# Kernel tuning notes

Hardware: AMD Instinct MI355X
Metric: run time of the kernel (lower is better)

## Reference

```python
import jax, jax.numpy as jnp
import numpy as np

N = 50000
E = 800000
G = 64
H, C = 16, 4  # heads, out_channels per head; H*C = 64


def setup_inputs() -> dict:
    key = jax.random.key(0)
    ks = jax.random.split(key, 16)
    return {
        "x": jax.random.normal(ks[0], (N,), jnp.float32),
        "edge_index": jax.random.randint(ks[1], (2, E), 0, N),
        "edge_attr": jax.random.normal(ks[2], (E,), jnp.float32),
        "batch": jnp.sort(jax.random.randint(ks[3], (N,), 0, G)),
        # GATv2Conv(1 -> 4, heads=16, edge_dim=1, concat=True)
        "Wl": jax.random.normal(ks[4], (1, H * C), jnp.float32) * 0.5,
        "bl": jnp.full((H * C,), 0.01, jnp.float32),
        "Wr": jax.random.normal(ks[5], (1, H * C), jnp.float32) * 0.5,
        "br": jnp.full((H * C,), 0.01, jnp.float32),
        "We": jax.random.normal(ks[6], (1, H * C), jnp.float32) * 0.5,
        "att": jax.random.normal(ks[7], (H, C), jnp.float32) * 0.5,
        "gat_bias": jnp.zeros((H * C,), jnp.float32),
        # GraphNorm(64)
        "gn_w": jnp.ones((H * C,), jnp.float32),
        "gn_b": jnp.zeros((H * C,), jnp.float32),
        "gn_ms": jnp.ones((H * C,), jnp.float32),
        # SAGEConv(64 -> 64, mean aggr, root weight)
        "sage_Wl": jax.random.normal(ks[8], (H * C, 64), jnp.float32) * 0.125,
        "sage_bl": jnp.full((64,), 0.01, jnp.float32),
        "sage_Wr": jax.random.normal(ks[9], (H * C, 64), jnp.float32) * 0.125,
        # MLP head
        "fc1_W": jax.random.normal(ks[10], (128, 2048), jnp.float32) * 0.08,
        "fc1_b": jnp.full((2048,), 0.01, jnp.float32),
        "fc2_W": jax.random.normal(ks[11], (2048, 1024), jnp.float32) * 0.02,
        "fc2_b": jnp.full((1024,), 0.01, jnp.float32),
        "fc3_W": jax.random.normal(ks[12], (1024, 3), jnp.float32) * 0.03,
        "fc3_b": jnp.full((3,), 0.01, jnp.float32),
    }


def reference(x, edge_index, edge_attr, batch, Wl, bl, Wr, br, We, att, gat_bias,
              gn_w, gn_b, gn_ms, sage_Wl, sage_bl, sage_Wr,
              fc1_W, fc1_b, fc2_W, fc2_b, fc3_W, fc3_b):
    src0, dst0 = edge_index[0], edge_index[1]
    x1 = x[:, None]  # [N,1] (torch.unsqueeze(x, -1))
    # ---- GATv2Conv ----
    xl = (x1 @ Wl + bl).reshape(N, H, C)  # source-side (x_j, also the value)
    xr = (x1 @ Wr + br).reshape(N, H, C)  # target-side (x_i)
    # add self loops; fill_value='mean' -> per-node mean of incoming edge_attr
    deg_in = jax.ops.segment_sum(jnp.ones((E,), x.dtype), dst0, num_segments=N)
    loop_attr = jax.ops.segment_sum(edge_attr, dst0, num_segments=N) / jnp.maximum(deg_in, 1.0)
    loops = jnp.arange(N)
    src = jnp.concatenate([src0, loops])
    dst = jnp.concatenate([dst0, loops])
    ea = jnp.concatenate([edge_attr, loop_attr])[:, None]  # [E+N,1]
    e = (ea @ We).reshape(-1, H, C)
    m = jax.nn.leaky_relu(xl[src] + xr[dst] + e, 0.2)  # [E+N,H,C]
    score = jnp.einsum('ehc,hc->eh', m, att)
    smax = jax.ops.segment_max(score, dst, num_segments=N)
    a = jnp.exp(score - smax[dst])
    denom = jax.ops.segment_sum(a, dst, num_segments=N)
    alpha = a / denom[dst]  # segmented softmax over incoming edges
    h = jax.ops.segment_sum(alpha[:, :, None] * xl[src], dst, num_segments=N)
    h = h.reshape(N, H * C) + gat_bias
    h = jax.nn.relu(h)
    # ---- GraphNorm ----
    cnt = jax.ops.segment_sum(jnp.ones((N,), x.dtype), batch, num_segments=G)[:, None]
    mean = jax.ops.segment_sum(h, batch, num_segments=G) / cnt
    o = h - mean[batch] * gn_ms
    var = jax.ops.segment_sum(o * o, batch, num_segments=G) / cnt
    h = gn_w * o / jnp.sqrt(var[batch] + 1e-5) + gn_b
    # ---- SAGEConv (mean aggregation + root weight) ----
    neigh = jax.ops.segment_sum(h[src0], dst0, num_segments=N) / jnp.maximum(deg_in, 1.0)[:, None]
    h = neigh @ sage_Wl + sage_bl + h @ sage_Wr
    h = jax.nn.relu(h)
    # ---- global max + mean pooling, MLP head (eval mode: dropout off) ----
    gmax = jax.ops.segment_max(h, batch, num_segments=G)
    gmean = jax.ops.segment_sum(h, batch, num_segments=G) / cnt
    g = jnp.concatenate([gmax, gmean], axis=1)  # [G, 128]
    g = jax.nn.relu(g @ fc1_W + fc1_b)
    g = jax.nn.relu(g @ fc2_W + fc2_b)
    return g @ fc3_W + fc3_b
```

## Files before the change

kernel.cpp:

```cpp
#include <hip/hip_runtime.h>

#define GG 64
#define HH 16
#define KK 64

__device__ __forceinline__ float bf2f(unsigned short u){
  return __uint_as_float(((unsigned)u) << 16);
}
__device__ __forceinline__ unsigned short f2bf(float f){
  unsigned u = __float_as_uint(f);
  unsigned r = u + 0x7fffu + ((u >> 16) & 1u);
  return (unsigned short)(r >> 16);
}

__global__ void k_zero(int4* __restrict__ p, int nInt4,
                       const int* __restrict__ batch, int N, int* __restrict__ goff){
  int t = blockIdx.x*blockDim.x + threadIdx.x;
  for (int i = t; i < nInt4; i += gridDim.x*blockDim.x)
    p[i] = make_int4(0,0,0,0);
  if (blockIdx.x == 0 && threadIdx.x <= GG){
    int g = threadIdx.x;
    int lo = 0, hi = N;
    while (lo < hi){ int mid = (lo+hi) >> 1; if (batch[mid] < g) lo = mid+1; else hi = mid; }
    goff[g] = lo;
  }
}


__global__ void k_count_rank(const int* __restrict__ ei, int* deg, int* __restrict__ rank, int E){
  int e = blockIdx.x*blockDim.x + threadIdx.x;
  if (e < E) rank[e] = atomicAdd(&deg[ei[E + e]], 1);
}

__global__ void k_scanA(const int* __restrict__ deg, int* __restrict__ bsum,
                        int* __restrict__ counter, int* __restrict__ row_start_N,
                        int N, int NB){
  int tid = threadIdx.x;
  int base = blockIdx.x*1024;
  int lim = min(base + 1024, N);
  int s = 0;
  for (int i = base + tid; i < lim; i += 256) s += deg[i];
  #pragma unroll
  for (int ofs = 32; ofs >= 1; ofs >>= 1) s += __shfl_down(s, ofs, 64);
  __shared__ int ws[4];
  __shared__ int lastflag;
  int lane = tid & 63, wv = tid >> 6;
  if (lane == 0) ws[wv] = s;
  __syncthreads();
  if (tid == 0){
    bsum[blockIdx.x] = ws[0] + ws[1] + ws[2] + ws[3];
    __threadfence();
    int d = atomicAdd(counter, 1);
    lastflag = (d == NB - 1);
  }
  __syncthreads();
  if (!lastflag) return;
  __threadfence();
  if (NB <= 64){
    if (tid < 64){
      int v = (tid < NB) ? bsum[tid] : 0;
      int val = v;
      #pragma unroll
      for (int ofs = 1; ofs < 64; ofs <<= 1){
        int tt = __shfl_up(val, ofs, 64);
        if ((tid & 63) >= ofs) val += tt;
      }
      if (tid < NB) bsum[tid] = val - v;
      if (tid == NB - 1) *row_start_N = val;
    }
  } else if (tid == 0){
    int run = 0;
    for (int i = 0; i < NB; ++i){ int tmp = bsum[i]; bsum[i] = run; run += tmp; }
    *row_start_N = run;
  }
}

__global__ void k_scan3(const int* __restrict__ deg, const int* __restrict__ bsum,
                        int* __restrict__ row_start, int N){
  int b = blockIdx.x;
  int base = b*1024 + (int)threadIdx.x*4;
  int d0 = (base+0 < N) ? deg[base+0] : 0;
  int d1 = (base+1 < N) ? deg[base+1] : 0;
  int d2 = (base+2 < N) ? deg[base+2] : 0;
  int d3 = (base+3 < N) ? deg[base+3] : 0;
  int s = d0 + d1 + d2 + d3;
  int lane = threadIdx.x & 63, wv = threadIdx.x >> 6;
  int val = s;
  #pragma unroll
  for (int ofs = 1; ofs < 64; ofs <<= 1){
    int tt = __shfl_up(val, ofs, 64);
    if (lane >= ofs) val += tt;
  }
  __shared__ int ws[4];
  if (lane == 63) ws[wv] = val;
  __syncthreads();
  if (threadIdx.x == 0){
    int run = 0;
    #pragma unroll
    for (int w = 0; w < 4; ++w){ int tmp = ws[w]; ws[w] = run; run += tmp; }
  }
  __syncthreads();
  int pre = bsum[b] + ws[wv] + val - s;
  if (base+0 < N){ row_start[base+0] = pre; pre += d0; }
  if (base+1 < N){ row_start[base+1] = pre; pre += d1; }
  if (base+2 < N){ row_start[base+2] = pre; pre += d2; }
  if (base+3 < N){ row_start[base+3] = pre; }
}

__global__ void k_scatter(const int* __restrict__ ei, const float* __restrict__ ea,
                          const int* __restrict__ row_start, const int* __restrict__ rank,
                          unsigned* __restrict__ cs, int E){
  int e = blockIdx.x*blockDim.x + threadIdx.x;
  if (e >= E) return;
  int d = ei[E + e];
  int pos = row_start[d] + rank[e];
  cs[pos] = ((unsigned)ei[e] & 0xFFFFu) | ((unsigned)f2bf(ea[e]) << 16);
}

__global__ void k_gat(const float* __restrict__ x, const int* __restrict__ row_start,
                      const unsigned* __restrict__ cs,
                      const float* __restrict__ Wl, const float* __restrict__ bl,
                      const float* __restrict__ Wr, const float* __restrict__ br,
                      const float* __restrict__ We, const float* __restrict__ att,
                      const float* __restrict__ gat_bias, const int* __restrict__ batch,
                      float* __restrict__ h, float* __restrict__ gsum, float* __restrict__ gsum2,
                      int N){
  __shared__ float sh[32][KK+1];
  __shared__ int bg[32];
  int tid = threadIdx.x;
  int t = blockIdx.x*blockDim.x + tid;
  int n   = t >> 3;
  int sub = t & 7;
  int u   = tid >> 3;
  bool act = (n < N);
  if (sub == 0) bg[u] = act ? batch[n] : -1;
  int k0 = sub*8;
  if (act){
    float xd = x[n];
    float wl[8], we[8], at[8], pre[8];
    #pragma unroll
    for (int i = 0; i < 8; ++i){
      int k = k0 + i;
      wl[i] = Wl[k]; we[i] = We[k]; at[i] = att[k];
      pre[i] = bl[k] + fmaf(xd, Wr[k], br[k]);
    }
    int e0 = row_start[n], e1 = row_start[n+1];
    float m[2]  = {-3.4e38f,-3.4e38f};
    float den[2] = {0,0}, S1[2] = {0,0};
    float asum = 0.f;

#define PROC(XS, EAV)                                                        \
    { float xs_ = (XS), ea_ = (EAV);                                         \
      _Pragma("unroll")                                                      \
      for (int hi2 = 0; hi2 < 2; ++hi2){                                     \
        float sc = 0.f;                                                      \
        _Pragma("unroll")                                                    \
        for (int c = 0; c < 4; ++c){                                         \
          int i = hi2*4 + c;                                                 \
          float tt = fmaf(xs_, wl[i], fmaf(ea_, we[i], pre[i]));             \
          tt = (tt > 0.f) ? tt : 0.2f*tt;                                    \
          sc = fmaf(tt, at[i], sc);                                          \
        }                                                                    \
        float nm = fmaxf(m[hi2], sc);                                        \
        float corr = __expf(m[hi2] - nm);                                    \
        float a    = __expf(sc - nm);                                        \
        den[hi2] = den[hi2]*corr + a;                                        \
        S1[hi2]  = S1[hi2] *corr + a*xs_;                                    \
        m[hi2] = nm; } }

    int e = e0;
    for (; e + 3 < e1; e += 4){
      unsigned w0 = cs[e], w1 = cs[e+1], w2 = cs[e+2], w3 = cs[e+3];
      float xs0 = x[w0 & 0xFFFFu], xs1 = x[w1 & 0xFFFFu];
      float xs2 = x[w2 & 0xFFFFu], xs3 = x[w3 & 0xFFFFu];
      float ea0 = bf2f((unsigned short)(w0 >> 16)), ea1 = bf2f((unsigned short)(w1 >> 16));
      float ea2 = bf2f((unsigned short)(w2 >> 16)), ea3 = bf2f((unsigned short)(w3 >> 16));
      asum += (ea0 + ea1) + (ea2 + ea3);
      PROC(xs0, ea0);
      PROC(xs1, ea1);
      PROC(xs2, ea2);
      PROC(xs3, ea3);
    }
    for (; e < e1; ++e){
      unsigned w0 = cs[e];
      float xs0 = x[w0 & 0xFFFFu], ea0 = bf2f((unsigned short)(w0 >> 16));
      asum += ea0;
      PROC(xs0, ea0);
    }
    {
      float degf = (float)(e1 - e0);
      float eav = asum / fmaxf(degf, 1.0f);
      PROC(xd, eav);
    }
#undef PROC
    #pragma unroll
    for (int hi2 = 0; hi2 < 2; ++hi2){
      float r = S1[hi2] / den[hi2];
      float4 o;
      #pragma unroll
      for (int c = 0; c < 4; ++c){
        int i = hi2*4 + c, k = k0 + i;
        float v = fmaxf(fmaf(wl[i], r, bl[k] + gat_bias[k]), 0.f);
        ((float*)&o)[c] = v;
        sh[u][k] = v;
      }
      *(float4*)(h + (size_t)n*KK + k0 + hi2*4) = o;
    }
  } else {
    #pragma unroll
    for (int i = 0; i < 8; ++i) sh[u][k0+i] = 0.f;
  }
  __syncthreads();
  int ch = tid & 63, slice = tid >> 6;
  int cg = -2; float rs = 0.f, rs2 = 0.f;
  for (int uu = slice*8; uu < slice*8 + 8; ++uu){
    int g = bg[uu];
    if (g != cg){
      if (cg >= 0){ atomicAdd(&gsum[cg*KK + ch], rs); atomicAdd(&gsum2[cg*KK + ch], rs2); }
      cg = g; rs = 0.f; rs2 = 0.f;
    }
    if (g >= 0){ float v = sh[uu][ch]; rs += v; rs2 += v*v; }
  }
  if (cg >= 0){ atomicAdd(&gsum[cg*KK + ch], rs); atomicAdd(&gsum2[cg*KK + ch], rs2); }
}

__global__ void k_norm(float* __restrict__ h, unsigned short* __restrict__ hb,
                       const int* __restrict__ batch,
                       const float* __restrict__ gsum, const float* __restrict__ gsum2,
                       const int* __restrict__ goff,
                       const float* __restrict__ gn_w, const float* __restrict__ gn_b,
                       const float* __restrict__ gn_ms, int N){
  int t = blockIdx.x*blockDim.x + threadIdx.x;
  if (t >= N*16) return;
  int n = t >> 4, q = t & 15;
  int b = batch[n];
  float c = fmaxf((float)(goff[b+1] - goff[b]), 1.0f);
  float inv = 1.0f / c;
  float4 hv = *(float4*)(h + (size_t)n*KK + q*4);
  float ov[4];
  #pragma unroll
  for (int i = 0; i < 4; ++i){
    int k = q*4 + i;
    float mean = gsum[b*KK + k]*inv;
    float eh2  = gsum2[b*KK + k]*inv;
    float ms = gn_ms[k];
    float var = eh2 - 2.f*ms*mean*mean + ms*ms*mean*mean;
    float sc = gn_w[k] * __frsqrt_rn(var + 1e-5f);
    float sh = gn_b[k] - sc*mean*ms;
    ov[i] = fmaf(sc, ((float*)&hv)[i], sh);
  }
  *(float4*)(h + (size_t)n*KK + q*4) = make_float4(ov[0], ov[1], ov[2], ov[3]);
  ushort4 bv;
  bv.x = f2bf(ov[0]); bv.y = f2bf(ov[1]); bv.z = f2bf(ov[2]); bv.w = f2bf(ov[3]);
  *(ushort4*)(hb + (size_t)n*KK + q*4) = bv;
}

__global__ void k_sage(const float* __restrict__ h, const unsigned short* __restrict__ hb,
                       const int* __restrict__ row_start, const unsigned* __restrict__ cs,
                       const float* __restrict__ Wl, const float* __restrict__ bln,
                       const float* __restrict__ Wr, const int* __restrict__ batch,
                       unsigned* __restrict__ gmaxu, float* __restrict__ gsumP, int N){
  __shared__ float snm[16][KK], shn[16][KK];
  __shared__ int bg[16];
  const ushort4* hb4 = (const ushort4*)hb;
  int tid = threadIdx.x;
  int u = tid >> 4;
  int q = tid & 15;
  int n = blockIdx.x*16 + u;
  if (tid < 16) bg[tid] = (blockIdx.x*16 + tid < N) ? batch[blockIdx.x*16 + tid] : -1;
  if (n < N){
    int e0 = row_start[n], e1 = row_start[n+1];
    float a0=0.f,a1=0.f,a2=0.f,a3=0.f;
    float b0=0.f,b1=0.f,b2=0.f,b3=0.f;
    int e = e0;
    for (; e + 7 < e1; e += 8){
      int s0 = cs[e]   & 0xFFFF, s1 = cs[e+1] & 0xFFFF, s2 = cs[e+2] & 0xFFFF, s3 = cs[e+3] & 0xFFFF;
      int s4 = cs[e+4] & 0xFFFF, s5 = cs[e+5] & 0xFFFF, s6 = cs[e+6] & 0xFFFF, s7 = cs[e+7] & 0xFFFF;
      ushort4 v0 = hb4[(size_t)s0*16 + q];
      ushort4 v1 = hb4[(size_t)s1*16 + q];
      ushort4 v2 = hb4[(size_t)s2*16 + q];
      ushort4 v3 = hb4[(size_t)s3*16 + q];
      ushort4 v4 = hb4[(size_t)s4*16 + q];
      ushort4 v5 = hb4[(size_t)s5*16 + q];
      ushort4 v6 = hb4[(size_t)s6*16 + q];
      ushort4 v7 = hb4[(size_t)s7*16 + q];
      a0 += bf2f(v0.x); a1 += bf2f(v0.y); a2 += bf2f(v0.z); a3 += bf2f(v0.w);
      b0 += bf2f(v1.x); b1 += bf2f(v1.y); b2 += bf2f(v1.z); b3 += bf2f(v1.w);
      a0 += bf2f(v2.x); a1 += bf2f(v2.y); a2 += bf2f(v2.z); a3 += bf2f(v2.w);
      b0 += bf2f(v3.x); b1 += bf2f(v3.y); b2 += bf2f(v3.z); b3 += bf2f(v3.w);
      a0 += bf2f(v4.x); a1 += bf2f(v4.y); a2 += bf2f(v4.z); a3 += bf2f(v4.w);
      b0 += bf2f(v5.x); b1 += bf2f(v5.y); b2 += bf2f(v5.z); b3 += bf2f(v5.w);
      a0 += bf2f(v6.x); a1 += bf2f(v6.y); a2 += bf2f(v6.z); a3 += bf2f(v6.w);
      b0 += bf2f(v7.x); b1 += bf2f(v7.y); b2 += bf2f(v7.z); b3 += bf2f(v7.w);
    }
    if (e + 3 < e1){
      int s0 = cs[e] & 0xFFFF, s1 = cs[e+1] & 0xFFFF, s2 = cs[e+2] & 0xFFFF, s3 = cs[e+3] & 0xFFFF;
      ushort4 v0 = hb4[(size_t)s0*16 + q];
      ushort4 v1 = hb4[(size_t)s1*16 + q];
      ushort4 v2 = hb4[(size_t)s2*16 + q];
      ushort4 v3 = hb4[(size_t)s3*16 + q];
      a0 += bf2f(v0.x); a1 += bf2f(v0.y); a2 += bf2f(v0.z); a3 += bf2f(v0.w);
      b0 += bf2f(v1.x); b1 += bf2f(v1.y); b2 += bf2f(v1.z); b3 += bf2f(v1.w);
      a0 += bf2f(v2.x); a1 += bf2f(v2.y); a2 += bf2f(v2.z); a3 += bf2f(v2.w);
      b0 += bf2f(v3.x); b1 += bf2f(v3.y); b2 += bf2f(v3.z); b3 += bf2f(v3.w);
      e += 4;
    }
    for (; e < e1; ++e){
      ushort4 v0 = hb4[(size_t)(cs[e] & 0xFFFF)*16 + q];
      a0 += bf2f(v0.x); a1 += bf2f(v0.y); a2 += bf2f(v0.z); a3 += bf2f(v0.w);
    }
    float dg = fmaxf((float)(e1 - e0), 1.0f);
    float inv = 1.0f/dg;
    float4 nm = make_float4((a0+b0)*inv, (a1+b1)*inv, (a2+b2)*inv, (a3+b3)*inv);
    *(float4*)&snm[u][q*4] = nm;
    *(float4*)&shn[u][q*4] = *(const float4*)(h + (size_t)n*KK + q*4);
  }
  __syncthreads();
  int j = tid & 63, u0 = tid >> 6;
  float acc[4];
  #pragma unroll
  for (int p = 0; p < 4; ++p) acc[p] = bln[j];
  for (int k = 0; k < KK; ++k){
    float wlv = Wl[k*KK + j], wrv = Wr[k*KK + j];
    #pragma unroll
    for (int p = 0; p < 4; ++p){
      int un = u0 + p*4;
      acc[p] = fmaf(snm[un][k], wlv, acc[p]);
      acc[p] = fmaf(shn[un][k], wrv, acc[p]);
    }
  }
  __syncthreads();
  #pragma unroll
  for (int p = 0; p < 4; ++p)
    snm[u0 + p*4][j] = fmaxf(acc[p], 0.f);
  __syncthreads();
  if (tid < 64){
    int cg = -2; float rmax = 0.f, rsum = 0.f;
    for (int uu = 0; uu < 16; ++uu){
      int g = bg[uu];
      if (g != cg){
        if (cg >= 0){
          atomicMax(&gmaxu[cg*KK + tid], __float_as_uint(rmax));
          atomicAdd(&gsumP[cg*KK + tid], rsum);
        }
        cg = g; rmax = 0.f; rsum = 0.f;
      }
      if (g >= 0){ float v = snm[uu][tid]; rmax = fmaxf(rmax, v); rsum += v; }
    }
    if (cg >= 0){
      atomicMax(&gmaxu[cg*KK + tid], __float_as_uint(rmax));
      atomicAdd(&gsumP[cg*KK + tid], rsum);
    }
  }
}


__global__ void k_fc1(const unsigned* __restrict__ gmaxu, const float* __restrict__ gsumP,
                      const int* __restrict__ goff,
                      const float* __restrict__ W, const float* __restrict__ b,
                      float* __restrict__ out){
  __shared__ float sin[128];
  int g = blockIdx.y, jt = blockIdx.x;
  int tid = threadIdx.x;
  if (tid < 128){
    float c = fmaxf((float)(goff[g+1] - goff[g]), 1.0f);
    sin[tid] = (tid < 64) ? __uint_as_float(gmaxu[g*64 + tid])
                          : gsumP[g*64 + (tid-64)] / c;
  }
  __syncthreads();
  int j = jt*256 + tid;
  float acc = b[j];
  #pragma unroll 16
  for (int k = 0; k < 128; ++k)
    acc = fmaf(sin[k], W[(size_t)k*2048 + j], acc);
  out[(size_t)g*2048 + j] = fmaxf(acc, 0.f);
}

__global__ void k_fc2a(const float* __restrict__ in, const float* __restrict__ W,
                       float* __restrict__ partial){
  __shared__ float sin[64][128];
  int jt = blockIdx.x, ks = blockIdx.y;
  int k0 = ks*128;
  int tid = threadIdx.x;
  for (int idx = tid; idx < 64*128; idx += 256){
    int g = idx >> 7, k = idx & 127;
    sin[g][k] = in[(size_t)g*2048 + k0 + k];
  }
  __syncthreads();
  int j = tid & 63, gs = tid >> 6;
  const float* Wp = W + (size_t)k0*1024 + jt*64 + j;
  float acc[16];
  #pragma unroll
  for (int p = 0; p < 16; ++p) acc[p] = 0.f;
  for (int k = 0; k < 128; ++k){
    float w = Wp[(size_t)k*1024];
    #pragma unroll
    for (int p = 0; p < 16; ++p)
      acc[p] = fmaf(sin[gs*16 + p][k], w, acc[p]);
  }
  #pragma unroll
  for (int p = 0; p < 16; ++p){
    int g = gs*16 + p;
    partial[((size_t)ks*64 + g)*1024 + jt*64 + j] = acc[p];
  }
}

__global__ void k_fc2red(const float* __restrict__ partial, const float* __restrict__ b,
                         float* __restrict__ out){
  int i = blockIdx.x*blockDim.x + threadIdx.x;
  int g = i >> 10, j = i & 1023;
  float s = b[j];
  #pragma unroll
  for (int ks = 0; ks < 16; ++ks)
    s += partial[((size_t)ks*64 + g)*1024 + j];
  out[i] = fmaxf(s, 0.f);
}

__global__ void k_fc3(const float* __restrict__ in, const float* __restrict__ W,
                      const float* __restrict__ b, float* __restrict__ out, int nOut){
  int w = (blockIdx.x*blockDim.x + threadIdx.x) >> 6;
  int lane = threadIdx.x & 63;
  if (w >= GG*nOut) return;
  int g = w / nOut, j = w - g*nOut;
  const float* row = in + (size_t)g*1024;
  float acc = 0.f;
  #pragma unroll
  for (int k = lane; k < 1024; k += 64)
    acc = fmaf(row[k], W[(size_t)k*nOut + j], acc);
  #pragma unroll
  for (int ofs = 32; ofs >= 1; ofs >>= 1)
    acc += __shfl_down(acc, ofs, 64);
  if (lane == 0) out[w] = acc + b[j];
}

extern "C" void kernel_launch(void* const* d_in, const int* in_sizes, int n_in,
                              void* d_out, int out_size, void* d_ws, size_t ws_size,
                              hipStream_t stream) {
  const float* x        = (const float*)d_in[0];
  const int*   ei       = (const int*)d_in[1];
  const float* ea       = (const float*)d_in[2];
  const int*   batch    = (const int*)d_in[3];
  const float* Wl       = (const float*)d_in[4];
  const float* bl       = (const float*)d_in[5];
  const float* Wr       = (const float*)d_in[6];
  const float* br       = (const float*)d_in[7];
  const float* We       = (const float*)d_in[8];
  const float* att      = (const float*)d_in[9];
  const float* gat_bias = (const float*)d_in[10];
  const float* gn_w     = (const float*)d_in[11];
  const float* gn_b     = (const float*)d_in[12];
  const float* gn_ms    = (const float*)d_in[13];
  const float* sage_Wl  = (const float*)d_in[14];
  const float* sage_bl  = (const float*)d_in[15];
  const float* sage_Wr  = (const float*)d_in[16];
  const float* fc1_W    = (const float*)d_in[17];
  const float* fc1_b    = (const float*)d_in[18];
  const float* fc2_W    = (const float*)d_in[19];
  const float* fc2_b    = (const float*)d_in[20];
  const float* fc3_W    = (const float*)d_in[21];
  const float* fc3_b    = (const float*)d_in[22];

  const int N = in_sizes[0];
  const int E = in_sizes[1] / 2;
  const int NB = (N + 1023) / 1024;

  char* ws = (char*)d_ws;
  size_t off = 0;
  auto alloc = [&](size_t bytes){ void* p = ws + off; off += (bytes + 255) & ~(size_t)255; return p; };

  int*      deg_i  = (int*)alloc((size_t)N*4);
  float*    gsum   = (float*)alloc(GG*KK*4);
  float*    gsum2  = (float*)alloc(GG*KK*4);
  unsigned* gmaxu  = (unsigned*)alloc(GG*KK*4);
  float*    gsumP  = (float*)alloc(GG*KK*4);
  int*      counter= (int*)alloc(256);
  size_t zero_bytes = off;
  int*   rank      = (int*)alloc((size_t)E*4);
  int*   bsum      = (int*)alloc((size_t)NB*4);
  int*   row_start = (int*)alloc((size_t)(N+1)*4);
  int*   goff      = (int*)alloc((GG+1)*4);
  unsigned* csp    = (unsigned*)alloc((size_t)E*4);
  float* h         = (float*)alloc((size_t)N*KK*4);
  unsigned short* hb = (unsigned short*)alloc((size_t)N*KK*2);
  float* out1      = (float*)alloc((size_t)GG*2048*4);
  float* out2      = (float*)alloc((size_t)GG*1024*4);
  float* partial   = (float*)alloc((size_t)16*GG*1024*4);
  (void)ws_size; (void)n_in; (void)out_size;

  const int B = 256;
  {
    int nInt4 = (int)(zero_bytes >> 4);
    int blocks = min((nInt4 + B - 1)/B, 256);
    k_zero <<<blocks, B, 0, stream>>>((int4*)d_ws, nInt4, batch, N, goff);
  }
  k_count_rank<<<(E+B-1)/B, B, 0, stream>>>(ei, deg_i, rank, E);
  k_scanA  <<<NB, B, 0, stream>>>(deg_i, bsum, counter, row_start + N, N, NB);
  k_scan3  <<<NB, B, 0, stream>>>(deg_i, bsum, row_start, N);
  k_scatter<<<(E+B-1)/B, B, 0, stream>>>(ei, ea, row_start, rank, csp, E);
  k_gat    <<<((size_t)N*8+B-1)/B, B, 0, stream>>>(x, row_start, csp,
                                                   Wl, bl, Wr, br, We, att, gat_bias,
                                                   batch, h, gsum, gsum2, N);
  k_norm   <<<((size_t)N*16+B-1)/B, B, 0, stream>>>(h, hb, batch, gsum, gsum2, goff,
                                                    gn_w, gn_b, gn_ms, N);
  k_sage   <<<(N+15)/16, B, 0, stream>>>(h, hb, row_start, csp, sage_Wl, sage_bl, sage_Wr,
                                         batch, gmaxu, gsumP, N);
  {
    dim3 grid(8, GG);
    k_fc1  <<<grid, 256, 0, stream>>>(gmaxu, gsumP, goff, fc1_W, fc1_b, out1);
  }
  {
    dim3 grid(16, 16);
    k_fc2a <<<grid, 256, 0, stream>>>(out1, fc2_W, partial);
  }
  k_fc2red <<<(GG*1024+B-1)/B, B, 0, stream>>>(partial, fc2_b, out2);
  k_fc3    <<<(GG*3*64+B-1)/B, B, 0, stream>>>(out2, fc3_W, fc3_b, (float*)d_out, 3);
}
```

Baseline: 179.2 us.

## Fuse scan into single-pass look-back and merge fc2 split-K with reduction

Replaces the two-kernel prefix scan with one kernel using a decoupled look-back over per-block status flags. Replaces the split-K fc2 plus separate reduction kernel with a single kernel that loops over the full K dimension and applies bias and ReLU in place. This removes two launches and the partial buffer traffic, but fc2 now runs only 64 blocks and re-reads the weight matrix once per group slice. The look-back also relies on forward progress of earlier blocks.

```diff
diff --git a/kernel.cpp b/kernel.cpp
--- a/kernel.cpp
+++ b/kernel.cpp
@@ -32,59 +32,17 @@
   if (e < E) rank[e] = atomicAdd(&deg[ei[E + e]], 1);
 }
 
-__global__ void k_scanA(const int* __restrict__ deg, int* __restrict__ bsum,
-                        int* __restrict__ counter, int* __restrict__ row_start_N,
-                        int N, int NB){
+__global__ void k_scanF(const int* __restrict__ deg, unsigned* __restrict__ status,
+                        int* __restrict__ row_start, int N, int NB){
+  int b = blockIdx.x;
   int tid = threadIdx.x;
-  int base = blockIdx.x*1024;
-  int lim = min(base + 1024, N);
-  int s = 0;
-  for (int i = base + tid; i < lim; i += 256) s += deg[i];
-  #pragma unroll
-  for (int ofs = 32; ofs >= 1; ofs >>= 1) s += __shfl_down(s, ofs, 64);
-  __shared__ int ws[4];
-  __shared__ int lastflag;
+  int base4 = b*1024 + tid*4;
+  int d0 = (base4+0 < N) ? deg[base4+0] : 0;
+  int d1 = (base4+1 < N) ? deg[base4+1] : 0;
+  int d2 = (base4+2 < N) ? deg[base4+2] : 0;
+  int d3 = (base4+3 < N) ? deg[base4+3] : 0;
+  int s = d0 + d1 + d2 + d3;
   int lane = tid & 63, wv = tid >> 6;
-  if (lane == 0) ws[wv] = s;
-  __syncthreads();
-  if (tid == 0){
-    bsum[blockIdx.x] = ws[0] + ws[1] + ws[2] + ws[3];
-    __threadfence();
-    int d = atomicAdd(counter, 1);
-    lastflag = (d == NB - 1);
-  }
-  __syncthreads();
-  if (!lastflag) return;
-  __threadfence();
-  if (NB <= 64){
-    if (tid < 64){
-      int v = (tid < NB) ? bsum[tid] : 0;
-      int val = v;
-      #pragma unroll
-      for (int ofs = 1; ofs < 64; ofs <<= 1){
-        int tt = __shfl_up(val, ofs, 64);
-        if ((tid & 63) >= ofs) val += tt;
-      }
-      if (tid < NB) bsum[tid] = val - v;
-      if (tid == NB - 1) *row_start_N = val;
-    }
-  } else if (tid == 0){
-    int run = 0;
-    for (int i = 0; i < NB; ++i){ int tmp = bsum[i]; bsum[i] = run; run += tmp; }
-    *row_start_N = run;
-  }
-}
-
-__global__ void k_scan3(const int* __restrict__ deg, const int* __restrict__ bsum,
-                        int* __restrict__ row_start, int N){
-  int b = blockIdx.x;
-  int base = b*1024 + (int)threadIdx.x*4;
-  int d0 = (base+0 < N) ? deg[base+0] : 0;
-  int d1 = (base+1 < N) ? deg[base+1] : 0;
-  int d2 = (base+2 < N) ? deg[base+2] : 0;
-  int d3 = (base+3 < N) ? deg[base+3] : 0;
-  int s = d0 + d1 + d2 + d3;
-  int lane = threadIdx.x & 63, wv = threadIdx.x >> 6;
   int val = s;
   #pragma unroll
   for (int ofs = 1; ofs < 64; ofs <<= 1){
@@ -92,19 +50,40 @@
     if (lane >= ofs) val += tt;
   }
   __shared__ int ws[4];
+  __shared__ int btot;
+  __shared__ int sbase;
   if (lane == 63) ws[wv] = val;
   __syncthreads();
-  if (threadIdx.x == 0){
+  if (tid == 0){
     int run = 0;
     #pragma unroll
     for (int w = 0; w < 4; ++w){ int tmp = ws[w]; ws[w] = run; run += tmp; }
-  }
-  __syncthreads();
-  int pre = bsum[b] + ws[wv] + val - s;
-  if (base+0 < N){ row_start[base+0] = pre; pre += d0; }
-  if (base+1 < N){ row_start[base+1] = pre; pre += d1; }
-  if (base+2 < N){ row_start[base+2] = pre; pre += d2; }
-  if (base+3 < N){ row_start[base+3] = pre; }
+    btot = run;
+    if (b == 0){
+      atomicExch(&status[0], ((unsigned)run << 2) | 2u);
+      sbase = 0;
+    } else {
+      atomicExch(&status[b], ((unsigned)run << 2) | 1u);
+      int acc = 0;
+      int i = b - 1;
+      while (true){
+        unsigned w;
+        do { w = atomicOr(&status[i], 0u); } while ((w & 3u) == 0u);
+        acc += (int)(w >> 2);
+        if ((w & 3u) == 2u) break;
+        --i;
+      }
+      sbase = acc;
+      atomicExch(&status[b], ((unsigned)(acc + run) << 2) | 2u);
+    }
+    if (b == NB - 1) row_start[N] = sbase + btot;
+  }
+  __syncthreads();
+  int pre = sbase + ws[wv] + val - s;
+  if (base4+0 < N){ row_start[base4+0] = pre; pre += d0; }
+  if (base4+1 < N){ row_start[base4+1] = pre; pre += d1; }
+  if (base4+2 < N){ row_start[base4+2] = pre; pre += d2; }
+  if (base4+3 < N){ row_start[base4+3] = pre; }
 }
 
 __global__ void k_scatter(const int* __restrict__ ei, const float* __restrict__ ea,
@@ -376,44 +355,34 @@
   out[(size_t)g*2048 + j] = fmaxf(acc, 0.f);
 }
 
-__global__ void k_fc2a(const float* __restrict__ in, const float* __restrict__ W,
-                       float* __restrict__ partial){
-  __shared__ float sin[64][128];
-  int jt = blockIdx.x, ks = blockIdx.y;
-  int k0 = ks*128;
+__global__ void k_fc2(const float* __restrict__ in, const float* __restrict__ W,
+                      const float* __restrict__ b, float* __restrict__ out){
+  __shared__ float sin[16][128];
+  int jt = blockIdx.x, gs = blockIdx.y;
   int tid = threadIdx.x;
-  for (int idx = tid; idx < 64*128; idx += 256){
-    int g = idx >> 7, k = idx & 127;
-    sin[g][k] = in[(size_t)g*2048 + k0 + k];
-  }
-  __syncthreads();
-  int j = tid & 63, gs = tid >> 6;
-  const float* Wp = W + (size_t)k0*1024 + jt*64 + j;
-  float acc[16];
-  #pragma unroll
-  for (int p = 0; p < 16; ++p) acc[p] = 0.f;
-  for (int k = 0; k < 128; ++k){
-    float w = Wp[(size_t)k*1024];
-    #pragma unroll
-    for (int p = 0; p < 16; ++p)
-      acc[p] = fmaf(sin[gs*16 + p][k], w, acc[p]);
-  }
-  #pragma unroll
-  for (int p = 0; p < 16; ++p){
-    int g = gs*16 + p;
-    partial[((size_t)ks*64 + g)*1024 + jt*64 + j] = acc[p];
-  }
-}
-
-__global__ void k_fc2red(const float* __restrict__ partial, const float* __restrict__ b,
-                         float* __restrict__ out){
-  int i = blockIdx.x*blockDim.x + threadIdx.x;
-  int g = i >> 10, j = i & 1023;
-  float s = b[j];
-  #pragma unroll
-  for (int ks = 0; ks < 16; ++ks)
-    s += partial[((size_t)ks*64 + g)*1024 + j];
-  out[i] = fmaxf(s, 0.f);
+  int j = jt*64 + (tid & 63);
+  int gslice = tid >> 6;
+  float acc[4] = {0.f,0.f,0.f,0.f};
+  for (int k0 = 0; k0 < 2048; k0 += 128){
+    for (int idx = tid; idx < 16*128; idx += 256){
+      int g = idx >> 7, k = idx & 127;
+      sin[g][k] = in[(size_t)(gs*16 + g)*2048 + k0 + k];
+    }
+    __syncthreads();
+    for (int k = 0; k < 128; ++k){
+      float w = W[(size_t)(k0 + k)*1024 + j];
+      #pragma unroll
+      for (int p = 0; p < 4; ++p)
+        acc[p] = fmaf(sin[gslice*4 + p][k], w, acc[p]);
+    }
+    __syncthreads();
+  }
+  float bj = b[j];
+  #pragma unroll
+  for (int p = 0; p < 4; ++p){
+    int g = gs*16 + gslice*4 + p;
+    out[(size_t)g*1024 + j] = fmaxf(acc[p] + bj, 0.f);
+  }
 }
 
 __global__ void k_fc3(const float* __restrict__ in, const float* __restrict__ W,
@@ -473,10 +442,9 @@
   float*    gsum2  = (float*)alloc(GG*KK*4);
   unsigned* gmaxu  = (unsigned*)alloc(GG*KK*4);
   float*    gsumP  = (float*)alloc(GG*KK*4);
-  int*      counter= (int*)alloc(256);
+  unsigned* status = (unsigned*)alloc((size_t)NB*4);
   size_t zero_bytes = off;
   int*   rank      = (int*)alloc((size_t)E*4);
-  int*   bsum      = (int*)alloc((size_t)NB*4);
   int*   row_start = (int*)alloc((size_t)(N+1)*4);
   int*   goff      = (int*)alloc((GG+1)*4);
   unsigned* csp    = (unsigned*)alloc((size_t)E*4);
@@ -484,7 +452,6 @@
   unsigned short* hb = (unsigned short*)alloc((size_t)N*KK*2);
   float* out1      = (float*)alloc((size_t)GG*2048*4);
   float* out2      = (float*)alloc((size_t)GG*1024*4);
-  float* partial   = (float*)alloc((size_t)16*GG*1024*4);
   (void)ws_size; (void)n_in; (void)out_size;
 
   const int B = 256;
@@ -494,8 +461,7 @@
     k_zero <<<blocks, B, 0, stream>>>((int4*)d_ws, nInt4, batch, N, goff);
   }
   k_count_rank<<<(E+B-1)/B, B, 0, stream>>>(ei, deg_i, rank, E);
-  k_scanA  <<<NB, B, 0, stream>>>(deg_i, bsum, counter, row_start + N, N, NB);
-  k_scan3  <<<NB, B, 0, stream>>>(deg_i, bsum, row_start, N);
+  k_scanF  <<<NB, B, 0, stream>>>(deg_i, status, row_start, N, NB);
   k_scatter<<<(E+B-1)/B, B, 0, stream>>>(ei, ea, row_start, rank, csp, E);
   k_gat    <<<((size_t)N*8+B-1)/B, B, 0, stream>>>(x, row_start, csp,
                                                    Wl, bl, Wr, br, We, att, gat_bias,
@@ -509,9 +475,8 @@
     k_fc1  <<<grid, 256, 0, stream>>>(gmaxu, gsumP, goff, fc1_W, fc1_b, out1);
   }
   {
-    dim3 grid(16, 16);
-    k_fc2a <<<grid, 256, 0, stream>>>(out1, fc2_W, partial);
-  }
-  k_fc2red <<<(GG*1024+B-1)/B, B, 0, stream>>>(partial, fc2_b, out2);
+    dim3 grid(16, 4);
+    k_fc2  <<<grid, 256, 0, stream>>>(out1, fc2_W, fc2_b, out2);
+  }
   k_fc3    <<<(GG*3*64+B-1)/B, B, 0, stream>>>(out2, fc3_W, fc3_b, (float*)d_out, 3);
 }
```

Result: slower. 276.4 us (+54.2%).
